# Optimization experiments

Hardware: AMD Instinct MI355X
Metric: run time of the kernel (lower is better)

The kernel has to match this reference:

```python
import jax, jax.numpy as jnp
import numpy as np

# dims: L=seq_len, B=batch, D=n_d (hidden), PROJ=n_proj, H=heads, DEPTH=layers, V=vocab
L, B, D, PROJ, H, DEPTH, V = 1024, 4, 1024, 256, 8, 4, 32000
HD = PROJ // H          # head dim = 32
NEG = -10000.0          # additive causal mask value used by Model.set_mask


def setup_inputs() -> dict:
    key = jax.random.key(0)
    ks = jax.random.split(key, 12)
    s = (3.0 / D) ** 0.5  # init used by Model.init_weights (layer_norm-style)
    return {
        "x": jax.random.randint(ks[0], (L, B), 0, V),
        "y": jax.random.randint(ks[1], (L, B), 0, V),
        "hidden": jnp.zeros((DEPTH, B, D), jnp.float32),            # init_hidden
        "emb_W": jax.random.uniform(ks[2], (V, D), jnp.float32, -s, s),
        # SRU++ attention transform per layer: q-proj, kv-proj, output to 3*D (U matrices)
        "W1": jax.random.normal(ks[3], (DEPTH, D, PROJ), jnp.float32) / np.float32(np.sqrt(D)),
        "W2": jax.random.normal(ks[4], (DEPTH, PROJ, 2 * PROJ), jnp.float32) / np.float32(np.sqrt(PROJ)),
        "W3": jax.random.normal(ks[5], (DEPTH, PROJ, 3 * D), jnp.float32) / np.float32(np.sqrt(PROJ)),
        "alpha": jax.random.normal(ks[6], (DEPTH,), jnp.float32) * 0.1,  # rezero scalar (nonzero so attn path is live)
        "weight_c": jax.random.normal(ks[7], (DEPTH, 2 * D), jnp.float32) * 0.1,  # (v_f, v_r)
        # bias = (b_f, b_r); forget bias initialized to highway_bias = -3
        "bias": jnp.concatenate([jnp.full((DEPTH, D), -3.0, jnp.float32), jnp.zeros((DEPTH, D), jnp.float32)], axis=-1),
        "Wout": jax.random.uniform(ks[8], (D, V), jnp.float32, -s, s),
        "bout": jnp.zeros((V,), jnp.float32),
    }


def _attention_transform(h, W1, W2, W3, alpha, mask):
    # SRUppAttention (no memory, no layer_norm, dropout=0)
    z = jnp.einsum('lbd,dp->lbp', h, W1)                 # (L,B,PROJ) query / residual
    kv = jnp.einsum('lbp,pq->lbq', z, W2)                # (L,B,2*PROJ)
    k, v = jnp.split(kv, 2, axis=-1)
    q = z.reshape(L, B, H, HD) * (HD ** -0.5)
    k = k.reshape(L, B, H, HD)
    v = v.reshape(L, B, H, HD)
    scores = jnp.einsum('lbhd,sbhd->bhls', q, k) + mask  # causal additive mask
    attn = jax.nn.softmax(scores, axis=-1)
    out = jnp.einsum('bhls,sbhd->lbhd', attn, v).reshape(L, B, PROJ)
    out = out * alpha + z                                # rezero residual
    return jnp.einsum('lbp,pk->lbk', out, W3)            # U: (L,B,3*D)


def _sru_recurrence(U, residual, c0, vf, vr, bf, br):
    # SRU elementwise highway recurrence (k=3, identity activation, no rescale)
    u = U.reshape(L, B, D, 3)
    u0 = u[..., 0]
    u1 = u[..., 1] + bf
    u2 = u[..., 2] + br

    def step(c, xs):
        u0t, u1t, u2t, rt = xs                           # each (B,D)
        f = jax.nn.sigmoid(u1t + vf * c)
        c = f * c + (1.0 - f) * u0t
        r = jax.nn.sigmoid(u2t + vr * c)
        h = r * c + (1.0 - r) * rt                       # highway on layer input
        return c, h

    c_last, hs = jax.lax.scan(step, c0, (u0, u1, u2, residual))
    return hs, c_last


def reference(x, y, hidden, emb_W, W1, W2, W3, alpha, weight_c, bias, Wout, bout):
    mask = jnp.triu(jnp.full((L, L), NEG, jnp.float32), 1)   # Model.set_mask, mem_len=0
    h = emb_W[x]                                             # (L,B,D) embedding lookup
    for i in range(DEPTH):
        U = _attention_transform(h, W1[i], W2[i], W3[i], alpha[i], mask)
        h, _ = _sru_recurrence(U, h, hidden[i],
                               weight_c[i, :D], weight_c[i, D:],
                               bias[i, :D], bias[i, D:])
    logits = jnp.einsum('lbd,dv->lbv', h, Wout) + bout       # (L,B,V)
    logp = jax.nn.log_softmax(logits, axis=-1)
    loss = -jnp.take_along_axis(logp, y[..., None], axis=-1)[..., 0]  # (L,B) per-token CE
    return loss
```

## Files before the change

kernel.cpp:

```cpp
#include <hip/hip_runtime.h>
#include <hip/hip_bf16.h>
#include <stdint.h>

#define L_ 1024
#define B_ 4
#define D_ 1024
#define PROJ_ 256
#define H_ 8
#define V_ 32000
#define M_ 4096

typedef __bf16 bf16x8 __attribute__((ext_vector_type(8)));
typedef float f32x4 __attribute__((ext_vector_type(4)));

#define AS3(p) ((__attribute__((address_space(3))) void*)(p))
#define AS1(p) ((const __attribute__((address_space(1))) void*)(p))

__global__ __launch_bounds__(256) void k_embed(const int* __restrict__ x,
                                               const float* __restrict__ emb,
                                               __hip_bfloat16* __restrict__ h) {
  int gid = blockIdx.x * 256 + threadIdx.x;
  int row = gid >> 8;
  int d0 = (gid & 255) << 2;
  int tok = x[row];
  const float4 v = *(const float4*)(emb + (size_t)tok * D_ + d0);
  union { __hip_bfloat16 o[4]; uint2 u; } cv;
  cv.o[0] = __float2bfloat16(v.x);
  cv.o[1] = __float2bfloat16(v.y);
  cv.o[2] = __float2bfloat16(v.z);
  cv.o[3] = __float2bfloat16(v.w);
  *(uint2*)(h + (size_t)row * D_ + d0) = cv.u;
}

__global__ __launch_bounds__(256) void k_transpose(const float* __restrict__ in,
                                                   __hip_bfloat16* __restrict__ out,
                                                   int K, int N,
                                                   long in_stride, long out_stride) {
  __shared__ float t[64][65];
  in += (size_t)blockIdx.z * in_stride;
  out += (size_t)blockIdx.z * out_stride;
  int n0 = blockIdx.x * 64, k0 = blockIdx.y * 64;
  int r = threadIdx.x >> 4, c4 = (threadIdx.x & 15) << 2;
#pragma unroll
  for (int p = 0; p < 4; p++) {
    float4 v = *(const float4*)(in + (size_t)(k0 + p * 16 + r) * N + n0 + c4);
    t[p * 16 + r][c4 + 0] = v.x;
    t[p * 16 + r][c4 + 1] = v.y;
    t[p * 16 + r][c4 + 2] = v.z;
    t[p * 16 + r][c4 + 3] = v.w;
  }
  __syncthreads();
  int n = threadIdx.x >> 2, kg = (threadIdx.x & 3) << 4;
  union { __hip_bfloat16 b[16]; uint4 u[2]; } cv;
#pragma unroll
  for (int i = 0; i < 16; i++) cv.b[i] = __float2bfloat16(t[kg + i][n]);
  uint4* op = (uint4*)(out + (size_t)(n0 + n) * K + k0 + kg);
  op[0] = cv.u[0];
  op[1] = cv.u[1];
}

template <bool CLS>
__global__ __launch_bounds__(256) void k_gemm_bt(
    const __hip_bfloat16* __restrict__ A, const __hip_bfloat16* __restrict__ Bt,
    __hip_bfloat16* __restrict__ C, int K, int N,
    const float* __restrict__ bout, const int* __restrict__ y,
    float2* __restrict__ lse, float* __restrict__ logitY) {
  __shared__ __hip_bfloat16 As[128 * 64];
  __shared__ __hip_bfloat16 Bs[128 * 64];
  const int tid = threadIdx.x;
  const int lane = tid & 63, wave = tid >> 6;
  const int quad = lane >> 4, l16 = lane & 15;
  const int wm = wave & 1, wn = wave >> 1;
  const int row0 = blockIdx.x * 128, col0 = blockIdx.y * 128;

  f32x4 acc[4][4] = {};

  const __hip_bfloat16* Abase = A + (size_t)row0 * K;
  const __hip_bfloat16* Bbase = Bt + (size_t)col0 * K;
  const int m_s = tid >> 3;
  const int ko_sw = (((tid & 7) ^ (m_s & 7)) << 3);
  const int xr = l16 & 7;

  for (int k0 = 0; k0 < K; k0 += 64) {
    __syncthreads();
#pragma unroll
    for (int call = 0; call < 4; call++) {
      int m = m_s + call * 32;
      __builtin_amdgcn_global_load_lds(AS1(Abase + (size_t)m * K + k0 + ko_sw),
                                       AS3(As + (call * 256 + wave * 64) * 8),
                                       16, 0, 0);
      __builtin_amdgcn_global_load_lds(AS1(Bbase + (size_t)m * K + k0 + ko_sw),
                                       AS3(Bs + (call * 256 + wave * 64) * 8),
                                       16, 0, 0);
    }
    __syncthreads();
#pragma unroll
    for (int kk = 0; kk < 2; kk++) {
      bf16x8 af[4], bfr[4];
#pragma unroll
      for (int mi = 0; mi < 4; mi++)
        af[mi] = *(const bf16x8*)(As + (wm * 64 + mi * 16 + l16) * 64 +
                                  (((kk * 4 + quad) ^ xr) << 3));
#pragma unroll
      for (int ni = 0; ni < 4; ni++)
        bfr[ni] = *(const bf16x8*)(Bs + (wn * 64 + ni * 16 + l16) * 64 +
                                   (((kk * 4 + quad) ^ xr) << 3));
#pragma unroll
      for (int mi = 0; mi < 4; mi++)
#pragma unroll
        for (int ni = 0; ni < 4; ni++)
          acc[mi][ni] = __builtin_amdgcn_mfma_f32_16x16x32_bf16(af[mi], bfr[ni],
                                                                acc[mi][ni], 0, 0, 0);
    }
  }

  if constexpr (!CLS) {
#pragma unroll
    for (int mi = 0; mi < 4; mi++)
#pragma unroll
      for (int ni = 0; ni < 4; ni++)
#pragma unroll
        for (int r = 0; r < 4; r++) {
          int row = row0 + wm * 64 + mi * 16 + quad * 4 + r;
          int col = col0 + wn * 64 + ni * 16 + l16;
          C[(size_t)row * N + col] = __float2bfloat16(acc[mi][ni][r]);
        }
  } else {
    const int chunk = blockIdx.y * 2 + wn;
    float bv[4];
#pragma unroll
    for (int ni = 0; ni < 4; ni++)
      bv[ni] = bout[col0 + wn * 64 + ni * 16 + l16];
#pragma unroll
    for (int mi = 0; mi < 4; mi++) {
#pragma unroll
      for (int r = 0; r < 4; r++) {
        int row = row0 + wm * 64 + mi * 16 + quad * 4 + r;
        float v0 = acc[mi][0][r] + bv[0];
        float v1 = acc[mi][1][r] + bv[1];
        float v2 = acc[mi][2][r] + bv[2];
        float v3 = acc[mi][3][r] + bv[3];
        int yv = y[row];
        int cb = col0 + wn * 64 + l16;
        if (yv == cb + 0)  logitY[row] = v0;
        if (yv == cb + 16) logitY[row] = v1;
        if (yv == cb + 32) logitY[row] = v2;
        if (yv == cb + 48) logitY[row] = v3;
        float m = fmaxf(fmaxf(v0, v1), fmaxf(v2, v3));
#pragma unroll
        for (int off = 1; off < 16; off <<= 1)
          m = fmaxf(m, __shfl_xor(m, off, 64));
        float s = __expf(v0 - m) + __expf(v1 - m) + __expf(v2 - m) + __expf(v3 - m);
#pragma unroll
        for (int off = 1; off < 16; off <<= 1)
          s += __shfl_xor(s, off, 64);
        if (l16 == 0)
          lse[(size_t)chunk * M_ + row] = make_float2(m, s);
      }
    }
  }
}

__global__ __launch_bounds__(256) void k_gemm_cls_f32(
    const __hip_bfloat16* __restrict__ A, const float* __restrict__ B,
    int K, int N, const float* __restrict__ bout, const int* __restrict__ y,
    float2* __restrict__ lse, float* __restrict__ logitY) {
  __shared__ __hip_bfloat16 As[128 * 40];
  __shared__ __hip_bfloat16 Bs[128 * 40];
  const int tid = threadIdx.x;
  const int lane = tid & 63, wave = tid >> 6;
  const int quad = lane >> 4, l16 = lane & 15;
  const int wm = wave & 1, wn = wave >> 1;
  const int row0 = blockIdx.x * 128, col0 = blockIdx.y * 128;
  f32x4 acc[4][4] = {};
  const int a_m = tid >> 1, a_k = (tid & 1) << 4;
  const int b_k = tid >> 3, b_n = (tid & 7) << 4;
  for (int k0 = 0; k0 < K; k0 += 32) {
    const uint4* ap = (const uint4*)(A + (size_t)(row0 + a_m) * K + k0 + a_k);
    uint4 av0 = ap[0];
    uint4 av1 = ap[1];
    const float* bp = B + (size_t)(k0 + b_k) * N + col0 + b_n;
    float4 bv0 = *(const float4*)(bp + 0);
    float4 bv1 = *(const float4*)(bp + 4);
    float4 bv2 = *(const float4*)(bp + 8);
    float4 bv3 = *(const float4*)(bp + 12);
    __syncthreads();
    *(uint4*)(As + a_m * 40 + a_k) = av0;
    *(uint4*)(As + a_m * 40 + a_k + 8) = av1;
    {
      float tmp[16] = {bv0.x, bv0.y, bv0.z, bv0.w, bv1.x, bv1.y, bv1.z, bv1.w,
                       bv2.x, bv2.y, bv2.z, bv2.w, bv3.x, bv3.y, bv3.z, bv3.w};
#pragma unroll
      for (int j = 0; j < 16; j++)
        Bs[(b_n + j) * 40 + b_k] = __float2bfloat16(tmp[j]);
    }
    __syncthreads();
    bf16x8 af[4], bfr[4];
#pragma unroll
    for (int mi = 0; mi < 4; mi++)
      af[mi] = *(const bf16x8*)(As + (wm * 64 + mi * 16 + l16) * 40 + quad * 8);
#pragma unroll
    for (int ni = 0; ni < 4; ni++)
      bfr[ni] = *(const bf16x8*)(Bs + (wn * 64 + ni * 16 + l16) * 40 + quad * 8);
#pragma unroll
    for (int mi = 0; mi < 4; mi++)
#pragma unroll
      for (int ni = 0; ni < 4; ni++)
        acc[mi][ni] = __builtin_amdgcn_mfma_f32_16x16x32_bf16(af[mi], bfr[ni],
                                                              acc[mi][ni], 0, 0, 0);
  }
  const int chunk = blockIdx.y * 2 + wn;
  float bv[4];
#pragma unroll
  for (int ni = 0; ni < 4; ni++)
    bv[ni] = bout[col0 + wn * 64 + ni * 16 + l16];
#pragma unroll
  for (int mi = 0; mi < 4; mi++) {
#pragma unroll
    for (int r = 0; r < 4; r++) {
      int row = row0 + wm * 64 + mi * 16 + quad * 4 + r;
      float v0 = acc[mi][0][r] + bv[0];
      float v1 = acc[mi][1][r] + bv[1];
      float v2 = acc[mi][2][r] + bv[2];
      float v3 = acc[mi][3][r] + bv[3];
      int yv = y[row];
      int cb = col0 + wn * 64 + l16;
      if (yv == cb + 0)  logitY[row] = v0;
      if (yv == cb + 16) logitY[row] = v1;
      if (yv == cb + 32) logitY[row] = v2;
      if (yv == cb + 48) logitY[row] = v3;
      float m = fmaxf(fmaxf(v0, v1), fmaxf(v2, v3));
#pragma unroll
      for (int off = 1; off < 16; off <<= 1)
        m = fmaxf(m, __shfl_xor(m, off, 64));
      float s = __expf(v0 - m) + __expf(v1 - m) + __expf(v2 - m) + __expf(v3 - m);
#pragma unroll
      for (int off = 1; off < 16; off <<= 1)
        s += __shfl_xor(s, off, 64);
      if (l16 == 0)
        lse[(size_t)chunk * M_ + row] = make_float2(m, s);
    }
  }
}

__global__ __launch_bounds__(256) void k_attn_mfma(
    const __hip_bfloat16* __restrict__ z, const __hip_bfloat16* __restrict__ kv,
    __hip_bfloat16* __restrict__ ao, const float* __restrict__ alpha_p) {
  __shared__ __hip_bfloat16 Qs[64 * 40];
  __shared__ __hip_bfloat16 Ks[128 * 40];
  __shared__ __hip_bfloat16 Vt[32 * 136];
  __shared__ __hip_bfloat16 Ps[64 * 136];
  const int tid = threadIdx.x;
  const int lane = tid & 63, wave = tid >> 6;
  const int quad = lane >> 4, l16 = lane & 15;
  const int bh = blockIdx.y, b = bh >> 3, h = bh & 7;
  const int q0 = blockIdx.x * 64;
  const float scale = 0.17677669529663687f;

  {
    int r = tid >> 2, c = (tid & 3) << 3;
    *(uint4*)(Qs + r * 40 + c) =
        *(const uint4*)(z + ((size_t)(q0 + r) * B_ + b) * PROJ_ + h * 32 + c);
  }

  float m_i[4] = {-1e30f, -1e30f, -1e30f, -1e30f};
  float l_i[4] = {0.f, 0.f, 0.f, 0.f};
  f32x4 o_acc[2] = {};

  const int ntile = (q0 + 191) >> 7;

  for (int t = 0; t < ntile; t++) {
    const int s0 = t << 7;
    __syncthreads();
    {
      int r = tid >> 1, c = (tid & 1) << 4;
      const uint4* kp =
          (const uint4*)(kv + ((size_t)(s0 + r) * B_ + b) * 512 + h * 32 + c);
      *(uint4*)(Ks + r * 40 + c) = kp[0];
      *(uint4*)(Ks + r * 40 + c + 8) = kp[1];
    }
    {
      int s = tid >> 1, dbase = (tid & 1) << 4;
      const __hip_bfloat16* vp =
          kv + ((size_t)(s0 + s) * B_ + b) * 512 + 256 + h * 32 + dbase;
      union { uint4 u; __hip_bfloat16 e[8]; } t0, t1;
      t0.u = *(const uint4*)vp;
      t1.u = *(const uint4*)(vp + 8);
#pragma unroll
      for (int j = 0; j < 8; j++) {
        Vt[(dbase + j) * 136 + s] = t0.e[j];
        Vt[(dbase + 8 + j) * 136 + s] = t1.e[j];
      }
    }
    __syncthreads();

    f32x4 sacc[8] = {};
    {
      bf16x8 aq = *(const bf16x8*)(Qs + (wave * 16 + l16) * 40 + quad * 8);
#pragma unroll
      for (int ni = 0; ni < 8; ni++) {
        bf16x8 bk = *(const bf16x8*)(Ks + (ni * 16 + l16) * 40 + quad * 8);
        sacc[ni] = __builtin_amdgcn_mfma_f32_16x16x32_bf16(aq, bk, sacc[ni], 0, 0, 0);
      }
    }

#pragma unroll
    for (int r = 0; r < 4; r++) {
      const int qrow = q0 + wave * 16 + quad * 4 + r;
      float mx = -1e30f;
#pragma unroll
      for (int ni = 0; ni < 8; ni++) {
        int s = s0 + ni * 16 + l16;
        float v = (s <= qrow) ? sacc[ni][r] * scale : -1e30f;
        sacc[ni][r] = v;
        mx = fmaxf(mx, v);
      }
#pragma unroll
      for (int off = 1; off < 16; off <<= 1)
        mx = fmaxf(mx, __shfl_xor(mx, off, 64));
      float mnew = fmaxf(m_i[r], mx);
      float al = __expf(m_i[r] - mnew);
      m_i[r] = mnew;
      float ps = 0.f;
#pragma unroll
      for (int ni = 0; ni < 8; ni++) {
        float p = __expf(sacc[ni][r] - mnew);
        Ps[(wave * 16 + quad * 4 + r) * 136 + ni * 16 + l16] = __float2bfloat16(p);
        ps += p;
      }
#pragma unroll
      for (int off = 1; off < 16; off <<= 1)
        ps += __shfl_xor(ps, off, 64);
      l_i[r] = l_i[r] * al + ps;
      o_acc[0][r] *= al;
      o_acc[1][r] *= al;
    }

#pragma unroll
    for (int ks = 0; ks < 4; ks++) {
      bf16x8 ap = *(const bf16x8*)(Ps + (wave * 16 + l16) * 136 + ks * 32 + quad * 8);
#pragma unroll
      for (int ni = 0; ni < 2; ni++) {
        bf16x8 bv = *(const bf16x8*)(Vt + (ni * 16 + l16) * 136 + ks * 32 + quad * 8);
        o_acc[ni] = __builtin_amdgcn_mfma_f32_16x16x32_bf16(ap, bv, o_acc[ni], 0, 0, 0);
      }
    }
  }

  const float arz = alpha_p[0];
#pragma unroll
  for (int ni = 0; ni < 2; ni++)
#pragma unroll
    for (int r = 0; r < 4; r++) {
      int row = q0 + wave * 16 + quad * 4 + r;
      size_t oi = ((size_t)row * B_ + b) * PROJ_ + h * 32 + ni * 16 + l16;
      float res = __bfloat162float(z[oi]);
      ao[oi] = __float2bfloat16(o_acc[ni][r] / l_i[r] * arz + res);
    }
}

__global__ __launch_bounds__(64) void k_sru(const __hip_bfloat16* __restrict__ U,
                                            __hip_bfloat16* __restrict__ h,
                                            const float* __restrict__ hidden,
                                            const float* __restrict__ wc,
                                            const float* __restrict__ bias) {
  int tid = blockIdx.x * 64 + threadIdx.x;
  int b = tid >> 10, d = tid & 1023;
  float vf = wc[d], vr = wc[D_ + d];
  float bfs = bias[d], brs = bias[D_ + d];
  float c = hidden[b * D_ + d];
  const __hip_bfloat16* up = U + (size_t)b * 3 * D_ + 3 * d;
  __hip_bfloat16* hp = h + (size_t)b * D_ + d;
  const int US = B_ * 3 * D_, HS = B_ * D_;
  for (int l0 = 0; l0 < L_; l0 += 8) {
    float u0[8], u1[8], u2[8], rs[8];
#pragma unroll
    for (int j = 0; j < 8; j++) {
      u0[j] = __bfloat162float(up[(size_t)j * US + 0]);
      u1[j] = __bfloat162float(up[(size_t)j * US + 1]);
      u2[j] = __bfloat162float(up[(size_t)j * US + 2]);
      rs[j] = __bfloat162float(hp[(size_t)j * HS]);
    }
#pragma unroll
    for (int j = 0; j < 8; j++) {
      float f = __builtin_amdgcn_rcpf(1.f + __expf(-(u1[j] + bfs + vf * c)));
      c = u0[j] + f * (c - u0[j]);
      float r = __builtin_amdgcn_rcpf(1.f + __expf(-(u2[j] + brs + vr * c)));
      hp[(size_t)j * HS] = __float2bfloat16(rs[j] + r * (c - rs[j]));
    }
    up += (size_t)8 * US;
    hp += (size_t)8 * HS;
  }
}

__global__ __launch_bounds__(256) void k_finalize(const float2* __restrict__ lse,
                                                  const float* __restrict__ logitY,
                                                  float* __restrict__ out) {
  int row = blockIdx.x * 256 + threadIdx.x;
  float M = -1e30f, S = 0.f;
  for (int c = 0; c < V_ / 64; c++) {
    float2 p = lse[(size_t)c * M_ + row];
    if (p.x > M) {
      S = S * __expf(M - p.x) + p.y;
      M = p.x;
    } else {
      S += p.y * __expf(p.x - M);
    }
  }
  out[row] = M + logf(S) - logitY[row];
}

extern "C" void kernel_launch(void* const* d_in, const int* in_sizes, int n_in,
                              void* d_out, int out_size, void* d_ws, size_t ws_size,
                              hipStream_t stream) {
  const int* x = (const int*)d_in[0];
  const int* y = (const int*)d_in[1];
  const float* hidden = (const float*)d_in[2];
  const float* emb = (const float*)d_in[3];
  const float* W1 = (const float*)d_in[4];
  const float* W2 = (const float*)d_in[5];
  const float* W3 = (const float*)d_in[6];
  const float* alpha = (const float*)d_in[7];
  const float* wc = (const float*)d_in[8];
  const float* bias = (const float*)d_in[9];
  const float* Wout = (const float*)d_in[10];
  const float* bout = (const float*)d_in[11];

  char* ws = (char*)d_ws;
  __hip_bfloat16* h16  = (__hip_bfloat16*)(ws + 0);
  __hip_bfloat16* z16  = (__hip_bfloat16*)(ws + 8388608);
  __hip_bfloat16* kv16 = (__hip_bfloat16*)(ws + 10485760);
  __hip_bfloat16* ao16 = (__hip_bfloat16*)(ws + 14680064);
  __hip_bfloat16* W1t  = (__hip_bfloat16*)(ws + 16777216);
  __hip_bfloat16* W2t  = (__hip_bfloat16*)(ws + 18874368);
  __hip_bfloat16* W3t  = (__hip_bfloat16*)(ws + 19922944);
  __hip_bfloat16* U16  = (__hip_bfloat16*)(ws + 26214400);
  const bool fast = ws_size >= 109723648ull;
  __hip_bfloat16* Woutt = (__hip_bfloat16*)(ws + 26214400);
  float2* lse    = (float2*)(ws + (fast ? 93323264u : 26214400u));
  float* logitY  = (float*)(ws + (fast ? 109707264u : 42598400u));
  float* out     = (float*)d_out;

  k_embed<<<4096, 256, 0, stream>>>(x, emb, h16);
  k_transpose<<<dim3(4, 16, 4), 256, 0, stream>>>(W1, W1t, D_, PROJ_,
                                                  (long)D_ * PROJ_, (long)PROJ_ * D_);
  k_transpose<<<dim3(8, 4, 4), 256, 0, stream>>>(W2, W2t, PROJ_, 2 * PROJ_,
                                                 (long)PROJ_ * 2 * PROJ_,
                                                 (long)2 * PROJ_ * PROJ_);
  k_transpose<<<dim3(48, 4, 4), 256, 0, stream>>>(W3, W3t, PROJ_, 3 * D_,
                                                  (long)PROJ_ * 3 * D_,
                                                  (long)3 * D_ * PROJ_);
  for (int i = 0; i < 4; i++) {
    k_gemm_bt<false><<<dim3(32, 2), 256, 0, stream>>>(
        h16, W1t + (size_t)i * PROJ_ * D_, z16, D_, PROJ_,
        nullptr, nullptr, nullptr, nullptr);
    k_gemm_bt<false><<<dim3(32, 4), 256, 0, stream>>>(
        z16, W2t + (size_t)i * 2 * PROJ_ * PROJ_, kv16, PROJ_, 2 * PROJ_,
        nullptr, nullptr, nullptr, nullptr);
    k_attn_mfma<<<dim3(16, 32), 256, 0, stream>>>(z16, kv16, ao16, alpha + i);
    k_gemm_bt<false><<<dim3(32, 24), 256, 0, stream>>>(
        ao16, W3t + (size_t)i * 3 * D_ * PROJ_, U16, PROJ_, 3 * D_,
        nullptr, nullptr, nullptr, nullptr);
    k_sru<<<64, 64, 0, stream>>>(U16, h16, hidden + (size_t)i * B_ * D_,
                                 wc + (size_t)i * 2 * D_, bias + (size_t)i * 2 * D_);
  }
  if (fast) {
    k_transpose<<<dim3(500, 16, 1), 256, 0, stream>>>(Wout, Woutt, D_, V_, 0, 0);
    k_gemm_bt<true><<<dim3(32, V_ / 128), 256, 0, stream>>>(
        h16, Woutt, nullptr, D_, V_, bout, y, lse, logitY);
  } else {
    k_gemm_cls_f32<<<dim3(32, V_ / 128), 256, 0, stream>>>(
        h16, Wout, D_, V_, bout, y, lse, logitY);
  }
  k_finalize<<<16, 256, 0, stream>>>(lse, logitY, out);
}
```

Baseline: 1.444 ms.

## Add 256x256-tile double-buffered classifier GEMM with direct-to-LDS loads

```diff
diff --git a/kernel.cpp b/kernel.cpp
--- a/kernel.cpp
+++ b/kernel.cpp
@@ -159,6 +159,170 @@
       }
     }
   }
+}
+
+__global__ __launch_bounds__(512, 2) void k_gemm_cls256(
+    const __hip_bfloat16* __restrict__ A, const __hip_bfloat16* __restrict__ Bt,
+    int K, const float* __restrict__ bout, const int* __restrict__ y,
+    float2* __restrict__ lse, float* __restrict__ logitY) {
+  __shared__ __align__(16) __hip_bfloat16 As[2][16384];
+  __shared__ __align__(16) __hip_bfloat16 Bs[2][16384];
+  const int tid = threadIdx.x;
+  const int lane = tid & 63, wave = tid >> 6;
+  const int quad = lane >> 4, l16 = lane & 15;
+  const int wm = wave >> 2, wn = wave & 3;
+
+  const int bid = blockIdx.y * 16 + blockIdx.x;
+  const int swzb = (bid & 7) * 250 + (bid >> 3);
+  const int bx = swzb & 15, by = swzb >> 4;
+  const int row0 = bx * 256, col0 = by * 256;
+
+  const int m_l = wave * 8 + (lane >> 3);
+  const int sw = ((lane & 7) ^ (lane >> 3)) << 3;
+  const __hip_bfloat16* Ag = A + (size_t)(row0 + m_l) * K + sw;
+  const __hip_bfloat16* Bg = Bt + (size_t)(col0 + m_l) * K + sw;
+
+#define STAGE_A(buf, r, ko)                                                   \
+  __builtin_amdgcn_global_load_lds(AS1(Ag + (size_t)(r) * 64 * K + (ko)),     \
+                                   AS3(&As[buf][((r) * 64 + wave * 8) * 64]), \
+                                   16, 0, 0)
+#define STAGE_B(buf, r, ko)                                                   \
+  __builtin_amdgcn_global_load_lds(AS1(Bg + (size_t)(r) * 64 * K + (ko)),     \
+                                   AS3(&Bs[buf][((r) * 64 + wave * 8) * 64]), \
+                                   16, 0, 0)
+
+  const int aoff = (wm * 128 + l16) * 64;
+  const int boff = (wn * 64 + l16) * 64;
+  const int cc0 = ((quad) ^ (l16 & 7)) << 3;
+  const int cc1 = ((4 + quad) ^ (l16 & 7)) << 3;
+
+  f32x4 acc[8][4] = {};
+  bf16x8 a4[4], b4[4];
+
+#define PH_PRE(buf, cck, mlo, READB)                                          \
+  do {                                                                        \
+    if (READB) {                                                              \
+      _Pragma("unroll") for (int ni = 0; ni < 4; ++ni)                        \
+          b4[ni] = *(const bf16x8*)(&Bs[buf][boff + ni * 1024 + (cck)]);      \
+    }                                                                         \
+    _Pragma("unroll") for (int mi = 0; mi < 4; ++mi)                          \
+        a4[mi] = *(const bf16x8*)(&As[buf][aoff + ((mlo) + mi) * 1024 + (cck)]); \
+  } while (0)
+
+#define PH_MFMA(mlo)                                                          \
+  do {                                                                        \
+    __builtin_amdgcn_s_barrier();                                             \
+    asm volatile("s_waitcnt lgkmcnt(0)" ::: "memory");                        \
+    __builtin_amdgcn_sched_barrier(0);                                        \
+    __builtin_amdgcn_s_setprio(1);                                            \
+    _Pragma("unroll") for (int mi = 0; mi < 4; ++mi)                          \
+        _Pragma("unroll") for (int ni = 0; ni < 4; ++ni)                      \
+            acc[(mlo) + mi][ni] = __builtin_amdgcn_mfma_f32_16x16x32_bf16(    \
+                a4[mi], b4[ni], acc[(mlo) + mi][ni], 0, 0, 0);                \
+    __builtin_amdgcn_s_setprio(0);                                            \
+  } while (0)
+
+#define BAR() __builtin_amdgcn_s_barrier()
+
+  STAGE_A(0, 0, 0); STAGE_A(0, 1, 0); STAGE_A(0, 2, 0); STAGE_A(0, 3, 0);
+  STAGE_B(0, 0, 0); STAGE_B(0, 1, 0); STAGE_B(0, 2, 0); STAGE_B(0, 3, 0);
+  STAGE_B(1, 0, 64); STAGE_B(1, 1, 64); STAGE_B(1, 2, 64); STAGE_B(1, 3, 64);
+  STAGE_A(1, 0, 64); STAGE_A(1, 2, 64);
+  asm volatile("s_waitcnt vmcnt(6)" ::: "memory");
+  BAR();
+
+  for (int i = 0; i < 7; ++i) {
+    const size_t kT1 = (size_t)i * 128 + 64;
+    const size_t kS0 = (size_t)i * 128 + 128;
+    const size_t kS1 = (size_t)i * 128 + 192;
+    PH_PRE(0, cc0, 0, 1);
+    STAGE_A(1, 1, kT1); STAGE_A(1, 3, kT1);
+    PH_MFMA(0); BAR();
+    PH_PRE(0, cc0, 4, 0);
+    PH_MFMA(4); BAR();
+    PH_PRE(0, cc1, 0, 1);
+    PH_MFMA(0); BAR();
+    PH_PRE(0, cc1, 4, 0);
+    STAGE_B(0, 0, kS0); STAGE_B(0, 1, kS0);
+    PH_MFMA(4);
+    asm volatile("s_waitcnt vmcnt(2)" ::: "memory");
+    BAR();
+    PH_PRE(1, cc0, 0, 1);
+    STAGE_B(0, 2, kS0); STAGE_B(0, 3, kS0);
+    PH_MFMA(0); BAR();
+    PH_PRE(1, cc0, 4, 0);
+    STAGE_A(0, 0, kS0); STAGE_A(0, 2, kS0);
+    PH_MFMA(4); BAR();
+    PH_PRE(1, cc1, 0, 1);
+    STAGE_A(0, 1, kS0); STAGE_A(0, 3, kS0);
+    PH_MFMA(0); BAR();
+    PH_PRE(1, cc1, 4, 0);
+    STAGE_B(1, 0, kS1); STAGE_B(1, 1, kS1); STAGE_B(1, 2, kS1); STAGE_B(1, 3, kS1);
+    STAGE_A(1, 0, kS1); STAGE_A(1, 2, kS1);
+    PH_MFMA(4);
+    asm volatile("s_waitcnt vmcnt(6)" ::: "memory");
+    BAR();
+  }
+  {
+    const size_t kT1 = (size_t)7 * 128 + 64;
+    PH_PRE(0, cc0, 0, 1);
+    STAGE_A(1, 1, kT1); STAGE_A(1, 3, kT1);
+    PH_MFMA(0); BAR();
+    PH_PRE(0, cc0, 4, 0);
+    PH_MFMA(4); BAR();
+    PH_PRE(0, cc1, 0, 1);
+    PH_MFMA(0); BAR();
+    PH_PRE(0, cc1, 4, 0);
+    PH_MFMA(4);
+    asm volatile("s_waitcnt vmcnt(0)" ::: "memory");
+    BAR();
+    PH_PRE(1, cc0, 0, 1);
+    PH_MFMA(0); BAR();
+    PH_PRE(1, cc0, 4, 0);
+    PH_MFMA(4); BAR();
+    PH_PRE(1, cc1, 0, 1);
+    PH_MFMA(0); BAR();
+    PH_PRE(1, cc1, 4, 0);
+    PH_MFMA(4);
+  }
+
+  const int chunk = by * 4 + wn;
+  float bv[4];
+#pragma unroll
+  for (int ni = 0; ni < 4; ++ni)
+    bv[ni] = bout[col0 + wn * 64 + ni * 16 + l16];
+#pragma unroll
+  for (int mi = 0; mi < 8; ++mi) {
+#pragma unroll
+    for (int r = 0; r < 4; ++r) {
+      int row = row0 + wm * 128 + mi * 16 + quad * 4 + r;
+      float v0 = acc[mi][0][r] + bv[0];
+      float v1 = acc[mi][1][r] + bv[1];
+      float v2 = acc[mi][2][r] + bv[2];
+      float v3 = acc[mi][3][r] + bv[3];
+      int yv = y[row];
+      int cb = col0 + wn * 64 + l16;
+      if (yv == cb + 0)  logitY[row] = v0;
+      if (yv == cb + 16) logitY[row] = v1;
+      if (yv == cb + 32) logitY[row] = v2;
+      if (yv == cb + 48) logitY[row] = v3;
+      float m = fmaxf(fmaxf(v0, v1), fmaxf(v2, v3));
+#pragma unroll
+      for (int off = 1; off < 16; off <<= 1)
+        m = fmaxf(m, __shfl_xor(m, off, 64));
+      float s = __expf(v0 - m) + __expf(v1 - m) + __expf(v2 - m) + __expf(v3 - m);
+#pragma unroll
+      for (int off = 1; off < 16; off <<= 1)
+        s += __shfl_xor(s, off, 64);
+      if (l16 == 0)
+        lse[(size_t)chunk * M_ + row] = make_float2(m, s);
+    }
+  }
+#undef STAGE_A
+#undef STAGE_B
+#undef PH_PRE
+#undef PH_MFMA
+#undef BAR
 }
 
 __global__ __launch_bounds__(256) void k_gemm_cls_f32(
@@ -466,8 +630,8 @@
   }
   if (fast) {
     k_transpose<<<dim3(500, 16, 1), 256, 0, stream>>>(Wout, Woutt, D_, V_, 0, 0);
-    k_gemm_bt<true><<<dim3(32, V_ / 128), 256, 0, stream>>>(
-        h16, Woutt, nullptr, D_, V_, bout, y, lse, logitY);
+    k_gemm_cls256<<<dim3(16, 125), 512, 0, stream>>>(h16, Woutt, D_, bout, y,
+                                                     lse, logitY);
   } else {
     k_gemm_cls_f32<<<dim3(32, V_ / 128), 256, 0, stream>>>(
         h16, Wout, D_, V_, bout, y, lse, logitY);
```

Measured after the change: 1.442 ms. Within noise of the previous version (-0.1%).
